# Kernel tuning notes

Hardware: AMD Instinct MI355X
Metric: run time of the kernel (lower is better)

Reference implementation:

```python
import jax, jax.numpy as jnp
import numpy as np

B, S, D, E, N, K = 4, 2048, 1024, 2048, 16, 4

def setup_inputs() -> dict:
    key = jax.random.key(0)
    ks = jax.random.split(key, 16)
    w = lambda k, shape, s=0.02: jax.random.normal(k, shape, dtype=jnp.float32) * s
    return {
        "x": jax.random.normal(ks[0], (B, S, D), dtype=jnp.float32),
        "ln_g": jnp.ones((D,), jnp.float32),
        "ln_b": jnp.zeros((D,), jnp.float32),
        "W_in": w(ks[1], (2 * E, D)),
        "b_in": jnp.zeros((2 * E,), jnp.float32),
        "conv_w": w(ks[2], (E, 1, K), 0.1),
        "conv_b": jnp.zeros((E,), jnp.float32),
        "A": w(ks[3], (E, N), 0.1),
        "Bm": w(ks[4], (E, N), 0.1),
        "W_c": w(ks[5], (E, E)),
        "b_c": jnp.zeros((E,), jnp.float32),
        "W_d": w(ks[6], (E, E)),
        "b_d": jnp.zeros((E,), jnp.float32),
        "log_delta": jnp.zeros((E,), jnp.float32),
        "W_out": w(ks[7], (D, E)),
        "b_out": jnp.zeros((D,), jnp.float32),
    }

def _layernorm(x, g, b, eps=1e-5):
    mu = jnp.mean(x, axis=-1, keepdims=True)
    var = jnp.var(x, axis=-1, keepdims=True)
    return (x - mu) * jax.lax.rsqrt(var + eps) * g + b

def _forward(x, ln_g, ln_b, W_in, b_in, conv_w, conv_b, A, Bm, W_c, b_c, W_d, b_d, log_delta, W_out, b_out):
    x_ln = _layernorm(x, ln_g, ln_b)
    x_proj = jnp.einsum("bsd,ed->bse", x_ln, W_in) + b_in  # (B,S,2E)
    xp, gate = jnp.split(x_proj, 2, axis=-1)
    # causal depthwise conv1d (torch pads K-1 both sides then truncates -> left pad only)
    xc = jax.lax.conv_general_dilated(
        xp.transpose(0, 2, 1), conv_w, (1,), [(K - 1, 0)],
        dimension_numbers=("NCH", "OIH", "NCH"), feature_group_count=E)
    xc = (xc + conv_b[None, :, None]).transpose(0, 2, 1)  # (B,S,E)
    xc = jax.nn.silu(xc)
    # selective SSM
    delta = jax.nn.softplus(log_delta)
    A_diag = jnp.exp(-delta)  # (E,)
    u = (jnp.einsum("bse,fe->bsf", xc, W_c) + b_c) * jax.nn.sigmoid(jnp.einsum("bse,fe->bsf", xc, W_d) + b_d)
    def step(h, u_t):
        # h: (B,E,N), u_t: (B,E)
        h = h * A_diag[None, :, None] + u_t[:, :, None] * Bm[None]
        y = jnp.sum(h * A[None], axis=-1)  # (B,E)
        return h, y
    h0 = jnp.zeros((x.shape[0], E, N), x.dtype)
    _, ys = jax.lax.scan(step, h0, u.transpose(1, 0, 2))  # ys: (S,B,E)
    x_ssm = ys.transpose(1, 0, 2)
    x_gated = x_ssm * jax.nn.sigmoid(gate)
    out = jnp.einsum("bse,de->bsd", x_gated, W_out) + b_out
    return out + x

def reference(x, ln_g, ln_b, W_in, b_in, conv_w, conv_b, A, Bm, W_c, b_c, W_d, b_d, log_delta, W_out, b_out):
    return _forward(x, ln_g, ln_b, W_in, b_in, conv_w, conv_b, A, Bm, W_c, b_c, W_d, b_d, log_delta, W_out, b_out)
```

## Files before the change

### kernel.cpp

```cpp
#include <hip/hip_runtime.h>
#include <hip/hip_bf16.h>

typedef __bf16 bf16_t;
typedef unsigned char u8;
typedef float  f32x4  __attribute__((ext_vector_type(4)));
typedef int    i32x4  __attribute__((ext_vector_type(4)));
typedef int    i32x8  __attribute__((ext_vector_type(8)));
typedef __attribute__((address_space(3))) unsigned as3u32;
typedef __attribute__((address_space(1))) unsigned as1u32;

#define Bdim 4
#define Sdim 2048
#define Ddim 1024
#define Edim 2048
#define CH 64
#define CL 32

#define WSCALE 32.0f
#define XPSCALE 32.0f
#define XCSCALE 16.0f
#define CSCALE 16.0f
#define GSCALE 256.0f

__device__ __forceinline__ void gload_lds16(const void* g, void* l) {
  __builtin_amdgcn_global_load_lds((const as1u32*)g, (as3u32*)l, 16, 0, 0);
}
__device__ __forceinline__ float sigmoidf_(float x) {
  return 1.f / (1.f + __expf(-x));
}
__device__ __forceinline__ int pk_fp8x4(float a, float b, float c, float d) {
  int p = __builtin_amdgcn_cvt_pk_fp8_f32(a, b, 0, 0);
  p = __builtin_amdgcn_cvt_pk_fp8_f32(c, d, p, 1);
  return p;
}
template<int K>
__device__ __forceinline__ float dq8(int v) {
  return __builtin_amdgcn_cvt_f32_fp8(v, K);
}
__device__ __forceinline__ u8 q8(float v) {
  return (u8)(__builtin_amdgcn_cvt_pk_fp8_f32(v, v, 0, 0) & 0xff);
}

__global__ __launch_bounds__(256)
void cvt_fp8_3(const float* __restrict__ s0, const float* __restrict__ s1,
               const float* __restrict__ s2, u8* __restrict__ d0,
               u8* __restrict__ d1, u8* __restrict__ d2) {
  const int seg = blockIdx.x >> 12;
  const int i   = ((blockIdx.x & 4095) * 256 + threadIdx.x) * 4;
  const float* s = (seg == 0) ? s0 : (seg == 1) ? s1 : s2;
  u8*          d = (seg == 0) ? d0 : (seg == 1) ? d1 : d2;
  *(int*)(d + i) = pk_fp8x4(s[i] * WSCALE, s[i + 1] * WSCALE,
                            s[i + 2] * WSCALE, s[i + 3] * WSCALE);
}

__global__ __launch_bounds__(256)
void cvt_fp8(const float* __restrict__ s, u8* __restrict__ d, int n, float scale) {
  int i = (blockIdx.x * 256 + threadIdx.x) * 4;
  if (i < n)
    *(int*)(d + i) = pk_fp8x4(s[i] * scale, s[i + 1] * scale,
                              s[i + 2] * scale, s[i + 3] * scale);
}

__global__ __launch_bounds__(256)
void prep_scalars(const float* __restrict__ ld, const float* __restrict__ Am,
                  const float* __restrict__ Bm, float* __restrict__ aexp,
                  float* __restrict__ Ce) {
  int e = blockIdx.x * 256 + threadIdx.x;
  if (e >= Edim) return;
  float d = ld[e];
  float sp = (d > 20.f) ? d : log1pf(expf(d));
  aexp[e] = expf(-sp);
  float s = 0.f;
  #pragma unroll
  for (int n = 0; n < 16; ++n) s += Am[e * 16 + n] * Bm[e * 16 + n];
  Ce[e] = s;
}

__global__ __launch_bounds__(256)
void ln_kernel(const float* __restrict__ x, const float* __restrict__ g,
               const float* __restrict__ b, u8* __restrict__ out) {
  const int row = blockIdx.x;
  const int tid = threadIdx.x;
  const float4 v = ((const float4*)(x + (size_t)row * Ddim))[tid];
  float s  = v.x + v.y + v.z + v.w;
  float ss = v.x * v.x + v.y * v.y + v.z * v.z + v.w * v.w;
  #pragma unroll
  for (int o = 32; o > 0; o >>= 1) { s += __shfl_down(s, o); ss += __shfl_down(ss, o); }
  __shared__ float sh[8];
  const int wv = tid >> 6, lane = tid & 63;
  if (lane == 0) { sh[wv] = s; sh[4 + wv] = ss; }
  __syncthreads();
  s  = sh[0] + sh[1] + sh[2] + sh[3];
  ss = sh[4] + sh[5] + sh[6] + sh[7];
  const float mean = s * (1.f / Ddim);
  const float var  = ss * (1.f / Ddim) - mean * mean;
  const float rstd = rsqrtf(var + 1e-5f);
  const float4 gv = ((const float4*)g)[tid];
  const float4 bv = ((const float4*)b)[tid];
  *(int*)(out + (size_t)row * Ddim + tid * 4) =
      pk_fp8x4((v.x - mean) * rstd * gv.x + bv.x,
               (v.y - mean) * rstd * gv.y + bv.y,
               (v.z - mean) * rstd * gv.z + bv.z,
               (v.w - mean) * rstd * gv.w + bv.w);
}

#define BM 128
#define BN 128

template<int MODE>
__global__ __launch_bounds__(256)
void gemm_mx(const u8* __restrict__ A, const u8* __restrict__ Bw,
             const float* __restrict__ bias, const u8* __restrict__ X,
             const float* __restrict__ R, u8* __restrict__ C8,
             float* __restrict__ Cf, float descale, float oscale,
             int M, int N, int K) {
  __shared__ __align__(16) u8 As[BM * 128];
  __shared__ __align__(16) u8 Bs[BN * 128];

  const int tid  = threadIdx.x;
  const int lane = tid & 63;
  const int wv   = tid >> 6;
  const int m0   = blockIdx.y * BM;
  const int n0   = blockIdx.x * BN;

  const int wr = (wv >> 1) * 64;
  const int wc = (wv & 1) * 64;
  const int tq = lane >> 4;
  const int tr = lane & 15;

  f32x4 acc[4][4] = {};

  size_t srcOff[4];
  int    ldsOff[4];
  #pragma unroll
  for (int g = 0; g < 4; ++g) {
    const int p   = g * 256 + tid;
    const int row = p >> 3;
    const int c   = (p & 7) ^ (row & 7);
    srcOff[g] = (size_t)row * K + c * 16;
    ldsOff[g] = g * 4096 + wv * 1024;
  }
  const size_t aBase = (size_t)m0 * K;
  const size_t bBase = (size_t)n0 * K;
  char* AsB = (char*)As;
  char* BsB = (char*)Bs;

  const int s7 = tr & 7;
  const int p0 = (((tq << 1)) ^ s7) * 16;
  const int p1 = (((tq << 1) | 1) ^ s7) * 16;

  for (int k0 = 0; k0 < K; k0 += 128) {
    __syncthreads();
    #pragma unroll
    for (int g = 0; g < 4; ++g)
      gload_lds16(A + aBase + srcOff[g] + k0, AsB + ldsOff[g]);
    #pragma unroll
    for (int g = 0; g < 4; ++g)
      gload_lds16(Bw + bBase + srcOff[g] + k0, BsB + ldsOff[g]);
    __syncthreads();

    i32x8 aF[4], bF[4];
    #pragma unroll
    for (int i = 0; i < 4; ++i) {
      const int rb = (wr + i * 16 + tr) * 128;
      const i32x4 lo = *(const i32x4*)&As[rb + p0];
      const i32x4 hi = *(const i32x4*)&As[rb + p1];
      aF[i] = __builtin_shufflevector(lo, hi, 0, 1, 2, 3, 4, 5, 6, 7);
    }
    #pragma unroll
    for (int j = 0; j < 4; ++j) {
      const int rb = (wc + j * 16 + tr) * 128;
      const i32x4 lo = *(const i32x4*)&Bs[rb + p0];
      const i32x4 hi = *(const i32x4*)&Bs[rb + p1];
      bF[j] = __builtin_shufflevector(lo, hi, 0, 1, 2, 3, 4, 5, 6, 7);
    }
    #pragma unroll
    for (int i = 0; i < 4; ++i)
      #pragma unroll
      for (int j = 0; j < 4; ++j)
        acc[i][j] = __builtin_amdgcn_mfma_scale_f32_16x16x128_f8f6f4(
            aF[i], bF[j], acc[i][j], 0, 0, 0, 0x7F, 0, 0x7F);
  }

  #pragma unroll
  for (int i = 0; i < 4; ++i) {
    #pragma unroll
    for (int j = 0; j < 4; ++j) {
      const int col = n0 + wc + j * 16 + tr;
      const float bv = bias[col];
      #pragma unroll
      for (int r = 0; r < 4; ++r) {
        const int rowg = m0 + wr + i * 16 + tq * 4 + r;
        const size_t idx = (size_t)rowg * N + col;
        const float v = acc[i][j][r] * descale + bv;
        if (MODE == 1) {
          Cf[idx] = v + R[idx];
        } else if (MODE == 2) {
          const float xv = dq8<0>((int)X[idx]);
          C8[idx] = q8(xv * sigmoidf_(v));
        } else {
          C8[idx] = q8(v * oscale);
        }
      }
    }
  }
}

#define BM2 256
#define BN2 256

template<int MODE>
__global__ __launch_bounds__(512, 2)
void gemm_mx2(const u8* __restrict__ A, const u8* __restrict__ Bw,
              const float* __restrict__ bias, const u8* __restrict__ X,
              u8* __restrict__ C8, float descale, float oscale,
              int M, int N, int K) {
  __shared__ __align__(16) u8 As[2][BM2 * 128];
  __shared__ __align__(16) u8 Bs[2][BN2 * 128];

  const int tid  = threadIdx.x;
  const int lane = tid & 63;
  const int wv   = tid >> 6;
  const int m0   = blockIdx.y * BM2;
  const int n0   = blockIdx.x * BN2;
  const int wr   = (wv >> 2) * 128;
  const int wc   = (wv & 3) * 64;
  const int tq   = lane >> 4;
  const int tr   = lane & 15;

  f32x4 acc[8][4] = {};

  const int    srow    = tid >> 3;
  const int    scol    = (tid & 7) ^ (srow & 7);
  const size_t sBase   = (size_t)srow * K + (size_t)scol * 16;
  const size_t rowStep = (size_t)64 * K;
  const u8* Ap = A  + (size_t)m0 * K + sBase;
  const u8* Bp = Bw + (size_t)n0 * K + sBase;
  const int ldsBase = wv * 1024;

  const int s7 = tr & 7;
  const int p0 = (((tq << 1)) ^ s7) * 16;
  const int p1 = (((tq << 1) | 1) ^ s7) * 16;

  const int NK = K >> 7;

  #pragma unroll
  for (int g = 0; g < 4; ++g)
    gload_lds16(Ap + g * rowStep, (u8*)As[0] + g * 8192 + ldsBase);
  #pragma unroll
  for (int g = 0; g < 4; ++g)
    gload_lds16(Bp + g * rowStep, (u8*)Bs[0] + g * 8192 + ldsBase);
  __syncthreads();

  for (int t = 0; t < NK; ++t) {
    const int cur = t & 1;
    if (t + 1 < NK) {
      const u8* An = Ap + (size_t)(t + 1) * 128;
      const u8* Bn = Bp + (size_t)(t + 1) * 128;
      #pragma unroll
      for (int g = 0; g < 4; ++g)
        gload_lds16(An + g * rowStep, (u8*)As[cur ^ 1] + g * 8192 + ldsBase);
      #pragma unroll
      for (int g = 0; g < 4; ++g)
        gload_lds16(Bn + g * rowStep, (u8*)Bs[cur ^ 1] + g * 8192 + ldsBase);
    }
    const u8* Ac = (const u8*)As[cur];
    const u8* Bc = (const u8*)Bs[cur];
    i32x8 aF[4], bF[4];
    #pragma unroll
    for (int j = 0; j < 4; ++j) {
      const int rb = (wc + j * 16 + tr) * 128;
      const i32x4 lo = *(const i32x4*)&Bc[rb + p0];
      const i32x4 hi = *(const i32x4*)&Bc[rb + p1];
      bF[j] = __builtin_shufflevector(lo, hi, 0, 1, 2, 3, 4, 5, 6, 7);
    }
    #pragma unroll
    for (int i = 0; i < 4; ++i) {
      const int rb = (wr + i * 16 + tr) * 128;
      const i32x4 lo = *(const i32x4*)&Ac[rb + p0];
      const i32x4 hi = *(const i32x4*)&Ac[rb + p1];
      aF[i] = __builtin_shufflevector(lo, hi, 0, 1, 2, 3, 4, 5, 6, 7);
    }
    __builtin_amdgcn_s_setprio(1);
    #pragma unroll
    for (int i = 0; i < 4; ++i)
      #pragma unroll
      for (int j = 0; j < 4; ++j)
        acc[i][j] = __builtin_amdgcn_mfma_scale_f32_16x16x128_f8f6f4(
            aF[i], bF[j], acc[i][j], 0, 0, 0, 0x7F, 0, 0x7F);
    __builtin_amdgcn_s_setprio(0);
    #pragma unroll
    for (int i = 0; i < 4; ++i) {
      const int rb = (wr + 64 + i * 16 + tr) * 128;
      const i32x4 lo = *(const i32x4*)&Ac[rb + p0];
      const i32x4 hi = *(const i32x4*)&Ac[rb + p1];
      aF[i] = __builtin_shufflevector(lo, hi, 0, 1, 2, 3, 4, 5, 6, 7);
    }
    __builtin_amdgcn_s_setprio(1);
    #pragma unroll
    for (int i = 0; i < 4; ++i)
      #pragma unroll
      for (int j = 0; j < 4; ++j)
        acc[4 + i][j] = __builtin_amdgcn_mfma_scale_f32_16x16x128_f8f6f4(
            aF[i], bF[j], acc[4 + i][j], 0, 0, 0, 0x7F, 0, 0x7F);
    __builtin_amdgcn_s_setprio(0);
    __syncthreads();
  }

  #pragma unroll
  for (int i = 0; i < 8; ++i) {
    #pragma unroll
    for (int j = 0; j < 4; ++j) {
      const int col = n0 + wc + j * 16 + tr;
      const float bv = bias[col];
      #pragma unroll
      for (int r = 0; r < 4; ++r) {
        const int rowg = m0 + wr + i * 16 + tq * 4 + r;
        const size_t idx = (size_t)rowg * N + col;
        const float v = acc[i][j][r] * descale + bv;
        if (MODE == 2) {
          const float xv = dq8<0>((int)X[idx]);
          C8[idx] = q8(xv * sigmoidf_(v));
        } else {
          C8[idx] = q8(v * oscale);
        }
      }
    }
  }
}

__global__ __launch_bounds__(256)
void conv_silu(const u8* __restrict__ xpg8, const float* __restrict__ cw,
               const float* __restrict__ cb, u8* __restrict__ xc8) {
  const int e0 = (blockIdx.y * 256 + threadIdx.x) * 4;
  const int b  = blockIdx.x >> 9;
  const int s0 = (blockIdx.x & 511) * 4;
  float w[4][4], bias[4];
  #pragma unroll
  for (int k = 0; k < 4; ++k) {
    const float4 wv = *(const float4*)(cw + (e0 + k) * 4);
    w[k][0] = wv.x; w[k][1] = wv.y; w[k][2] = wv.z; w[k][3] = wv.w;
    bias[k] = cb[e0 + k];
  }
  float f[7][4];
  #pragma unroll
  for (int j = 0; j < 7; ++j) {
    const int s = s0 - 3 + j;
    const int xv = (s >= 0) ? *(const int*)(xpg8 + (size_t)(b * Sdim + s) * (2 * Edim) + e0) : 0;
    f[j][0] = dq8<0>(xv); f[j][1] = dq8<1>(xv);
    f[j][2] = dq8<2>(xv); f[j][3] = dq8<3>(xv);
  }
  #pragma unroll
  for (int t = 0; t < 4; ++t) {
    float y[4];
    #pragma unroll
    for (int k = 0; k < 4; ++k) {
      float a = fmaf(w[k][0], f[t][k],
               fmaf(w[k][1], f[t + 1][k],
               fmaf(w[k][2], f[t + 2][k],
                    w[k][3] * f[t + 3][k])));
      a = a * (1.f / XPSCALE) + bias[k];
      y[k] = a * sigmoidf_(a) * XCSCALE;
    }
    *(int*)(xc8 + (size_t)(b * Sdim + s0 + t) * Edim + e0) =
        pk_fp8x4(y[0], y[1], y[2], y[3]);
  }
}

__global__ __launch_bounds__(256)
void scan_part1(const u8* __restrict__ u8p, const float* __restrict__ aexp,
                float* __restrict__ zloc) {
  const int c  = blockIdx.x;
  const int b  = blockIdx.y >> 1;
  const int e0 = ((blockIdx.y & 1) * 256 + threadIdx.x) * 4;
  const float4 av = *(const float4*)(aexp + e0);
  const u8* up = u8p + ((size_t)(b * Sdim + c * CL)) * Edim + e0;
  float z0 = 0.f, z1 = 0.f, z2 = 0.f, z3 = 0.f;
  #pragma unroll
  for (int t = 0; t < CL; ++t) {
    const int uv = *(const int*)(up + (size_t)t * Edim);
    z0 = fmaf(av.x, z0, dq8<0>(uv));
    z1 = fmaf(av.y, z1, dq8<1>(uv));
    z2 = fmaf(av.z, z2, dq8<2>(uv));
    z3 = fmaf(av.w, z3, dq8<3>(uv));
  }
  float4 zv = {z0, z1, z2, z3};
  *(float4*)(zloc + ((size_t)b * CH + c) * Edim + e0) = zv;
}

__global__ __launch_bounds__(256)
void scan_part2(const float* __restrict__ aexp, float* __restrict__ zloc) {
  const int idx = blockIdx.x * 256 + threadIdx.x;
  const int b = idx >> 11, e = idx & (Edim - 1);
  float a  = aexp[e];
  float aL = a * a;
  aL = aL * aL; aL = aL * aL; aL = aL * aL; aL = aL * aL;
  float* zp = zloc + (size_t)b * CH * Edim + e;
  float pref = 0.f;
  #pragma unroll 4
  for (int c = 0; c < CH; ++c) {
    const float loc = zp[(size_t)c * Edim];
    zp[(size_t)c * Edim] = pref;
    pref = fmaf(aL, pref, loc);
  }
}

__global__ __launch_bounds__(256)
void scan_part3(const u8* __restrict__ u8p, const u8* __restrict__ xpg8,
                const float* __restrict__ aexp, const float* __restrict__ Ce,
                const float* __restrict__ zloc, u8* __restrict__ xg8) {
  const int c  = blockIdx.x;
  const int b  = blockIdx.y >> 1;
  const int e0 = ((blockIdx.y & 1) * 256 + threadIdx.x) * 4;
  const float4 av = *(const float4*)(aexp + e0);
  float4 Cv = *(const float4*)(Ce + e0);
  const float cs = GSCALE / CSCALE;
  Cv.x *= cs; Cv.y *= cs; Cv.z *= cs; Cv.w *= cs;
  float4 zv = *(const float4*)(zloc + ((size_t)b * CH + c) * Edim + e0);
  const u8* up = u8p  + ((size_t)(b * Sdim + c * CL)) * Edim + e0;
  const u8* gp = xpg8 + ((size_t)(b * Sdim + c * CL)) * (2 * Edim) + Edim + e0;
  u8*       op = xg8  + ((size_t)(b * Sdim + c * CL)) * Edim + e0;
  #pragma unroll 4
  for (int t = 0; t < CL; ++t) {
    const int uv = *(const int*)(up + (size_t)t * Edim);
    const int gv = *(const int*)(gp + (size_t)t * (2 * Edim));
    zv.x = fmaf(av.x, zv.x, dq8<0>(uv));
    zv.y = fmaf(av.y, zv.y, dq8<1>(uv));
    zv.z = fmaf(av.z, zv.z, dq8<2>(uv));
    zv.w = fmaf(av.w, zv.w, dq8<3>(uv));
    const float y0 = Cv.x * zv.x * sigmoidf_(dq8<0>(gv) * (1.f / XPSCALE));
    const float y1 = Cv.y * zv.y * sigmoidf_(dq8<1>(gv) * (1.f / XPSCALE));
    const float y2 = Cv.z * zv.z * sigmoidf_(dq8<2>(gv) * (1.f / XPSCALE));
    const float y3 = Cv.w * zv.w * sigmoidf_(dq8<3>(gv) * (1.f / XPSCALE));
    *(int*)(op + (size_t)t * Edim) = pk_fp8x4(y0, y1, y2, y3);
  }
}

extern "C" void kernel_launch(void* const* d_in, const int* in_sizes, int n_in,
                              void* d_out, int out_size, void* d_ws, size_t ws_size,
                              hipStream_t stream) {
  const float* x         = (const float*)d_in[0];
  const float* ln_g      = (const float*)d_in[1];
  const float* ln_b      = (const float*)d_in[2];
  const float* W_in      = (const float*)d_in[3];
  const float* b_in      = (const float*)d_in[4];
  const float* conv_w    = (const float*)d_in[5];
  const float* conv_b    = (const float*)d_in[6];
  const float* Am        = (const float*)d_in[7];
  const float* Bm        = (const float*)d_in[8];
  const float* W_c       = (const float*)d_in[9];
  const float* b_c       = (const float*)d_in[10];
  const float* W_d       = (const float*)d_in[11];
  const float* b_d       = (const float*)d_in[12];
  const float* log_delta = (const float*)d_in[13];
  const float* W_out     = (const float*)d_in[14];
  const float* b_out     = (const float*)d_in[15];
  float* out = (float*)d_out;

  const size_t MiB = 1024 * 1024;
  char* w = (char*)d_ws;
  u8*     wWin8  = (u8*)   (w + 0);
  u8*     wWc8   = (u8*)   (w + 4 * MiB);
  u8*     wWd8   = (u8*)   (w + 8 * MiB);
  u8*     wWout8 = (u8*)   (w + 12 * MiB);
  float*  aexp   = (float*)(w + 15 * MiB);
  float*  Ce     = (float*)(w + 15 * MiB + 16384);
  float*  zloc   = (float*)(w + 15 * MiB + 65536);
  u8*     xln8   = (u8*)   (w + 18 * MiB);
  u8*     xpg8   = (u8*)   (w + 26 * MiB);
  u8*     xc8    = (u8*)   (w + 58 * MiB);
  u8*     c8     = (u8*)   (w + 74 * MiB);
  u8*     u8b    = (u8*)   (w + 90 * MiB);
  u8*     xg8    = (u8*)   (w + 106 * MiB);

  const int M = Bdim * Sdim;
  const float dsIn  = 1.f / WSCALE;
  const float dsCD  = 1.f / (WSCALE * XCSCALE);
  const float dsOut = 1.f / (WSCALE * GSCALE);

  cvt_fp8_3<<<3 * 4096, 256, 0, stream>>>(W_in, W_c, W_d, wWin8, wWc8, wWd8);
  cvt_fp8<<<(Ddim * Edim) / 1024, 256, 0, stream>>>(W_out, wWout8, Ddim * Edim, WSCALE);
  prep_scalars<<<Edim / 256, 256, 0, stream>>>(log_delta, Am, Bm, aexp, Ce);

  ln_kernel<<<M, 256, 0, stream>>>(x, ln_g, ln_b, xln8);

  gemm_mx2<3><<<dim3((2 * Edim) / BN2, M / BM2), 512, 0, stream>>>(
      xln8, wWin8, b_in, nullptr, xpg8, dsIn, XPSCALE, M, 2 * Edim, Ddim);

  conv_silu<<<dim3(Bdim * (Sdim / 4), Edim / 1024), 256, 0, stream>>>(xpg8, conv_w, conv_b, xc8);

  gemm_mx2<3><<<dim3(Edim / BN2, M / BM2), 512, 0, stream>>>(
      xc8, wWc8, b_c, nullptr, c8, dsCD, CSCALE, M, Edim, Edim);
  gemm_mx2<2><<<dim3(Edim / BN2, M / BM2), 512, 0, stream>>>(
      xc8, wWd8, b_d, c8, u8b, dsCD, 1.f, M, Edim, Edim);

  scan_part1<<<dim3(CH, Bdim * 2), 256, 0, stream>>>(u8b, aexp, zloc);
  scan_part2<<<(Bdim * Edim) / 256, 256, 0, stream>>>(aexp, zloc);
  scan_part3<<<dim3(CH, Bdim * 2), 256, 0, stream>>>(u8b, xpg8, aexp, Ce, zloc, xg8);

  gemm_mx<1><<<dim3(Ddim / BN, M / BM), 256, 0, stream>>>(
      xg8, wWout8, b_out, nullptr, x, nullptr, out, dsOut, 1.f, M, Ddim, Edim);

  (void)in_sizes; (void)n_in; (void)out_size; (void)ws_size;
}
```

Baseline: 380.1 us.

## Restructure fp8 GEMM mainloop into barrier-synced quadrant schedule with two-ahead prefetch

Rewrites the gemm_mx2 K loop to run two tiles per iteration, each on its own named LDS buffer pair. Each K tile is split into four MFMA quadrants, with fragment loads staged between them and s_barrier plus setprio used to keep waves in lockstep. Global-to-LDS loads now run two tiles ahead and are tracked with explicit vmcnt waits instead of __syncthreads. The goal is better overlap of LDS reads, global loads and MFMA work, at the cost of many more barriers. It also assumes the number of K tiles is even and relies on hand-counted vmcnt values.

```diff
diff --git a/kernel.cpp b/kernel.cpp
--- a/kernel.cpp
+++ b/kernel.cpp
@@ -209,14 +209,87 @@
 #define BM2 256
 #define BN2 256
 
+#define RDF(dst, P, rowe)                                                      \
+  {                                                                            \
+    const int rb_ = (rowe) * 128;                                              \
+    const i32x4 lo_ = *(const i32x4*)&(P)[rb_ + p0];                           \
+    const i32x4 hi_ = *(const i32x4*)&(P)[rb_ + p1];                           \
+    (dst) = __builtin_shufflevector(lo_, hi_, 0, 1, 2, 3, 4, 5, 6, 7);         \
+  }
+
+#define MM8(AF, BF, IO, JO)                                                    \
+  {                                                                            \
+    _Pragma("unroll") for (int i_ = 0; i_ < 4; ++i_)                           \
+      _Pragma("unroll") for (int j_ = 0; j_ < 2; ++j_)                         \
+        acc[(IO) + i_][(JO) + j_] =                                            \
+            __builtin_amdgcn_mfma_scale_f32_16x16x128_f8f6f4(                  \
+                (AF)[i_], (BF)[j_], acc[(IO) + i_][(JO) + j_],                 \
+                0, 0, 0, 0x7F, 0, 0x7F);                                       \
+  }
+
+#define KTILE(AS, BS, t_)                                                      \
+  {                                                                            \
+    i32x8 aLo[4], aHi[4], bLo[2], bHi[2];                                      \
+                                         \
+    RDF(bLo[0], BS, wc + tr);                                                  \
+    RDF(bLo[1], BS, wc + 16 + tr);                                             \
+    RDF(aLo[0], AS, wr + tr);                                                  \
+    RDF(aLo[1], AS, wr + 16 + tr);                                             \
+    RDF(aLo[2], AS, wr + 32 + tr);                                             \
+    RDF(aLo[3], AS, wr + 48 + tr);                                             \
+    __builtin_amdgcn_s_barrier();                                              \
+    __builtin_amdgcn_s_setprio(1);                                             \
+    MM8(aLo, bLo, 0, 0);                                                       \
+    __builtin_amdgcn_s_setprio(0);                                             \
+    __builtin_amdgcn_s_barrier();                                              \
+                               \
+    RDF(bHi[0], BS, wc + 32 + tr);                                             \
+    RDF(bHi[1], BS, wc + 48 + tr);                                             \
+    __builtin_amdgcn_s_barrier();                                              \
+    __builtin_amdgcn_s_setprio(1);                                             \
+    MM8(aLo, bHi, 0, 2);                                                       \
+    __builtin_amdgcn_s_setprio(0);                                             \
+    __builtin_amdgcn_s_barrier();                                              \
+                    \
+    RDF(aHi[0], AS, wr + 64 + tr);                                             \
+    RDF(aHi[1], AS, wr + 80 + tr);                                             \
+    RDF(aHi[2], AS, wr + 96 + tr);                                             \
+    RDF(aHi[3], AS, wr + 112 + tr);                                            \
+    __builtin_amdgcn_s_barrier();                                              \
+    __builtin_amdgcn_s_setprio(1);                                             \
+    MM8(aHi, bHi, 4, 2);                                                       \
+    __builtin_amdgcn_s_setprio(0);                                             \
+    __builtin_amdgcn_s_barrier();                                              \
+     \
+    if ((t_) + 2 < NK) {                                                       \
+      const size_t ko_ = (size_t)((t_) + 2) * 128;                             \
+      _Pragma("unroll") for (int g_ = 0; g_ < 4; ++g_)                         \
+        gload_lds16(Ap + g_ * rowStep + ko_, (u8*)(AS) + g_ * 8192 + ldsBase); \
+      _Pragma("unroll") for (int g_ = 0; g_ < 4; ++g_)                         \
+        gload_lds16(Bp + g_ * rowStep + ko_, (u8*)(BS) + g_ * 8192 + ldsBase); \
+    }                                                                          \
+    __builtin_amdgcn_s_setprio(1);                                             \
+    MM8(aHi, bLo, 4, 0);                                                       \
+    __builtin_amdgcn_s_setprio(0);                                             \
+     \
+    if ((t_) + 2 < NK) {                                                       \
+      asm volatile("s_waitcnt vmcnt(8)" ::: "memory");                         \
+    } else {                                                                   \
+      asm volatile("s_waitcnt vmcnt(0)" ::: "memory");                         \
+    }                                                                          \
+    __builtin_amdgcn_s_barrier();                                              \
+  }
+
 template<int MODE>
 __global__ __launch_bounds__(512, 2)
 void gemm_mx2(const u8* __restrict__ A, const u8* __restrict__ Bw,
               const float* __restrict__ bias, const u8* __restrict__ X,
               u8* __restrict__ C8, float descale, float oscale,
               int M, int N, int K) {
-  __shared__ __align__(16) u8 As[2][BM2 * 128];
-  __shared__ __align__(16) u8 Bs[2][BN2 * 128];
+  __shared__ __align__(16) u8 As0[BM2 * 128];
+  __shared__ __align__(16) u8 Bs0[BN2 * 128];
+  __shared__ __align__(16) u8 As1[BM2 * 128];
+  __shared__ __align__(16) u8 Bs1[BN2 * 128];
 
   const int tid  = threadIdx.x;
   const int lane = tid & 63;
@@ -246,65 +319,23 @@
 
   #pragma unroll
   for (int g = 0; g < 4; ++g)
-    gload_lds16(Ap + g * rowStep, (u8*)As[0] + g * 8192 + ldsBase);
+    gload_lds16(Ap + g * rowStep, (u8*)As0 + g * 8192 + ldsBase);
   #pragma unroll
   for (int g = 0; g < 4; ++g)
-    gload_lds16(Bp + g * rowStep, (u8*)Bs[0] + g * 8192 + ldsBase);
-  __syncthreads();
-
-  for (int t = 0; t < NK; ++t) {
-    const int cur = t & 1;
-    if (t + 1 < NK) {
-      const u8* An = Ap + (size_t)(t + 1) * 128;
-      const u8* Bn = Bp + (size_t)(t + 1) * 128;
-      #pragma unroll
-      for (int g = 0; g < 4; ++g)
-        gload_lds16(An + g * rowStep, (u8*)As[cur ^ 1] + g * 8192 + ldsBase);
-      #pragma unroll
-      for (int g = 0; g < 4; ++g)
-        gload_lds16(Bn + g * rowStep, (u8*)Bs[cur ^ 1] + g * 8192 + ldsBase);
-    }
-    const u8* Ac = (const u8*)As[cur];
-    const u8* Bc = (const u8*)Bs[cur];
-    i32x8 aF[4], bF[4];
-    #pragma unroll
-    for (int j = 0; j < 4; ++j) {
-      const int rb = (wc + j * 16 + tr) * 128;
-      const i32x4 lo = *(const i32x4*)&Bc[rb + p0];
-      const i32x4 hi = *(const i32x4*)&Bc[rb + p1];
-      bF[j] = __builtin_shufflevector(lo, hi, 0, 1, 2, 3, 4, 5, 6, 7);
-    }
-    #pragma unroll
-    for (int i = 0; i < 4; ++i) {
-      const int rb = (wr + i * 16 + tr) * 128;
-      const i32x4 lo = *(const i32x4*)&Ac[rb + p0];
-      const i32x4 hi = *(const i32x4*)&Ac[rb + p1];
-      aF[i] = __builtin_shufflevector(lo, hi, 0, 1, 2, 3, 4, 5, 6, 7);
-    }
-    __builtin_amdgcn_s_setprio(1);
-    #pragma unroll
-    for (int i = 0; i < 4; ++i)
-      #pragma unroll
-      for (int j = 0; j < 4; ++j)
-        acc[i][j] = __builtin_amdgcn_mfma_scale_f32_16x16x128_f8f6f4(
-            aF[i], bF[j], acc[i][j], 0, 0, 0, 0x7F, 0, 0x7F);
-    __builtin_amdgcn_s_setprio(0);
-    #pragma unroll
-    for (int i = 0; i < 4; ++i) {
-      const int rb = (wr + 64 + i * 16 + tr) * 128;
-      const i32x4 lo = *(const i32x4*)&Ac[rb + p0];
-      const i32x4 hi = *(const i32x4*)&Ac[rb + p1];
-      aF[i] = __builtin_shufflevector(lo, hi, 0, 1, 2, 3, 4, 5, 6, 7);
-    }
-    __builtin_amdgcn_s_setprio(1);
-    #pragma unroll
-    for (int i = 0; i < 4; ++i)
-      #pragma unroll
-      for (int j = 0; j < 4; ++j)
-        acc[4 + i][j] = __builtin_amdgcn_mfma_scale_f32_16x16x128_f8f6f4(
-            aF[i], bF[j], acc[4 + i][j], 0, 0, 0, 0x7F, 0, 0x7F);
-    __builtin_amdgcn_s_setprio(0);
-    __syncthreads();
+    gload_lds16(Bp + g * rowStep, (u8*)Bs0 + g * 8192 + ldsBase);
+  #pragma unroll
+  for (int g = 0; g < 4; ++g)
+    gload_lds16(Ap + g * rowStep + 128, (u8*)As1 + g * 8192 + ldsBase);
+  #pragma unroll
+  for (int g = 0; g < 4; ++g)
+    gload_lds16(Bp + g * rowStep + 128, (u8*)Bs1 + g * 8192 + ldsBase);
+  asm volatile("s_waitcnt vmcnt(8)" ::: "memory");
+  __builtin_amdgcn_s_barrier();
+
+  for (int tp = 0; tp < (NK >> 1); ++tp) {
+    const int t0 = tp * 2;
+    KTILE(As0, Bs0, t0);
+    KTILE(As1, Bs1, t0 + 1);
   }
 
   #pragma unroll
```

Result: slower. 785.7 us (+106.7%).
